# Optimization experiments

Measured on AMD Instinct MI355X. Metric: run time of the kernel, lower is better.

The kernel has to match this reference:

```python
import jax, jax.numpy as jnp
import numpy as np

B, L, F, H, DIM = 32, 1024, 1024, 1024, 1024


def setup_inputs() -> dict:
    key = jax.random.key(0)
    ks = jax.random.split(key, 8)
    features = jax.random.normal(ks[0], (B, L, F), dtype=jnp.float32)
    hidden = jax.random.normal(ks[1], (B, H), dtype=jnp.float32)
    # Dense layer params (glorot-ish scale)
    W1 = jax.random.normal(ks[2], (F, DIM), dtype=jnp.float32) / np.sqrt(F)
    b1 = jnp.zeros((DIM,), dtype=jnp.float32)
    W2 = jax.random.normal(ks[3], (H, DIM), dtype=jnp.float32) / np.sqrt(H)
    b2 = jnp.zeros((DIM,), dtype=jnp.float32)
    Wp = jax.random.normal(ks[4], (DIM, 1), dtype=jnp.float32) / np.sqrt(DIM)
    bp = jnp.zeros((1,), dtype=jnp.float32)
    return {"features": features, "hidden": hidden, "W1": W1, "b1": b1,
            "W2": W2, "b2": b2, "Wp": Wp, "bp": bp}


def reference(features, hidden, W1, b1, W2, b2, Wp, bp):
    # features: [B, L, F], hidden: [B, H]
    h1 = jnp.einsum('blf,fd->bld', features, W1) + b1          # [B, L, D]
    h2 = (hidden @ W2 + b2)[:, None, :]                         # [B, 1, D]
    att = jnp.tanh(h1 + h2)                                     # [B, L, D]
    score = jnp.einsum('bld,do->blo', att, Wp) + bp             # [B, L, 1]
    attention_weights = jax.nn.softmax(score, axis=1)           # [B, L, 1]
    context_vector = jnp.sum(attention_weights * features, axis=1)  # [B, F]
    return context_vector
```

## Files before the change

### kernel.cpp

```cpp
#include <hip/hip_runtime.h>
#include <hip/hip_bf16.h>


typedef __attribute__((ext_vector_type(8))) __bf16 bf16x8;
typedef __attribute__((ext_vector_type(4))) float f32x4;

#define BM 128
#define BN 128
#define BK 32
#define LDK 40

static __device__ __forceinline__ ushort f2bf(float x) {
  unsigned u = __float_as_uint(x);
  return (ushort)((u + 0x7fffu + ((u >> 16) & 1u)) >> 16);
}

typedef __attribute__((address_space(1))) void gbl_t;
typedef __attribute__((address_space(3))) void lds_t;
static __device__ __forceinline__ void gl_lds16(const void* g, void* l) {
  __builtin_amdgcn_global_load_lds((gbl_t*)g, (lds_t*)l, 16, 0, 0);
}

static __device__ __forceinline__ bf16x8 cvt8(float4 lo, float4 hi) {
  __hip_bfloat162 c0 = __float22bfloat162_rn({lo.x, lo.y});
  __hip_bfloat162 c1 = __float22bfloat162_rn({lo.z, lo.w});
  __hip_bfloat162 c2 = __float22bfloat162_rn({hi.x, hi.y});
  __hip_bfloat162 c3 = __float22bfloat162_rn({hi.z, hi.w});
  union { int4 i; bf16x8 v; } u;
  u.i.x = *(int*)&c0; u.i.y = *(int*)&c1; u.i.z = *(int*)&c2; u.i.w = *(int*)&c3;
  return u.v;
}

__global__ __launch_bounds__(256) void cvt_feat_kernel(
    const float* __restrict__ feat, ushort* __restrict__ featb) {
  const size_t i8 = ((size_t)blockIdx.x * 256 + threadIdx.x) * 8;
  float4 a = *(const float4*)(feat + i8);
  float4 b = *(const float4*)(feat + i8 + 4);
  ushort t[8];
  t[0] = f2bf(a.x); t[1] = f2bf(a.y); t[2] = f2bf(a.z); t[3] = f2bf(a.w);
  t[4] = f2bf(b.x); t[5] = f2bf(b.y); t[6] = f2bf(b.z); t[7] = f2bf(b.w);
  *(int4*)(featb + i8) = *(int4*)t;
}

__global__ __launch_bounds__(256) void transpose_w1_kernel(
    const float* __restrict__ W1, ushort* __restrict__ W1T) {
  __shared__ float t[64][65];
  const int tr = blockIdx.y, tc = blockIdx.x, tid = threadIdx.x;
  const int r = tid >> 4;
  const int c4 = (tid & 15) * 4;
#pragma unroll
  for (int p = 0; p < 4; ++p) {
    const int rr = p * 16 + r;
    float4 v = *(const float4*)(W1 + (size_t)(tr * 64 + rr) * 1024 + tc * 64 + c4);
    t[rr][c4] = v.x; t[rr][c4 + 1] = v.y; t[rr][c4 + 2] = v.z; t[rr][c4 + 3] = v.w;
  }
  __syncthreads();
  const int cc = tid >> 3;
  const int r8 = (tid & 7) * 8;
#pragma unroll
  for (int p = 0; p < 2; ++p) {
    const int c = p * 32 + cc;
    ushort tmp[8];
#pragma unroll
    for (int j = 0; j < 8; ++j) tmp[j] = f2bf(t[r8 + j][c]);
    *(int4*)(W1T + (size_t)(tc * 64 + c) * 1024 + tr * 64 + r8) = *(int4*)tmp;
  }
}

__global__ void zero_kernel(float* __restrict__ p) {
  p[(size_t)blockIdx.x * 256 + threadIdx.x] = 0.f;
}

__global__ __launch_bounds__(256) void h2_kernel(
    const float* __restrict__ hidden, const float* __restrict__ W2,
    const float* __restrict__ b2, float* __restrict__ h2p) {
  const int d = blockIdx.x * 256 + threadIdx.x;
  const int b = blockIdx.y;
  const int z = blockIdx.z;
  const int k0 = z * 128;
  __shared__ float h[128];
  if (threadIdx.x < 128) h[threadIdx.x] = hidden[b * 1024 + k0 + threadIdx.x];
  __syncthreads();
  float acc = (z == 0) ? b2[d] : 0.f;
#pragma unroll 8
  for (int k = 0; k < 128; ++k)
    acc += h[k] * W2[(size_t)(k0 + k) * 1024 + d];
  h2p[z * 32768 + b * 1024 + d] = acc;
}

#define GEMM_EPILOGUE(ROWG)                                                    \
  float hbv[4], wpv[4];                                                        \
  _Pragma("unroll") for (int j = 0; j < 4; ++j) {                              \
    const int d = col0 + wn * 64 + j * 16 + lrow;                              \
    float hv = b1[d];                                                          \
    _Pragma("unroll") for (int p = 0; p < 8; ++p)                              \
        hv += h2p[p * 32768 + b * 1024 + d];                                   \
    hbv[j] = hv;                                                               \
    wpv[j] = wp[d];                                                            \
  }                                                                            \
  float rsum[4][4];                                                            \
  _Pragma("unroll") for (int i = 0; i < 4; ++i) {                              \
    _Pragma("unroll") for (int r = 0; r < 4; ++r) {                            \
      float s = 0.f;                                                           \
      _Pragma("unroll") for (int j = 0; j < 4; ++j)                            \
          s += tanhf(acc[i][j][r] + hbv[j]) * wpv[j];                          \
      s += __shfl_xor(s, 8);                                                   \
      s += __shfl_xor(s, 4);                                                   \
      s += __shfl_xor(s, 2);                                                   \
      s += __shfl_xor(s, 1);                                                   \
      rsum[i][r] = s;                                                          \
    }                                                                          \
  }                                                                            \
  if (wn == 1 && lrow == 0) {                                                  \
    _Pragma("unroll") for (int i = 0; i < 4; ++i)                              \
        _Pragma("unroll") for (int r = 0; r < 4; ++r)                          \
            sred[wm][i * 16 + quad * 4 + r] = rsum[i][r];                      \
  }                                                                            \
  __syncthreads();                                                             \
  if (wn == 0 && lrow == 0) {                                                  \
    _Pragma("unroll") for (int i = 0; i < 4; ++i)                              \
        _Pragma("unroll") for (int r = 0; r < 4; ++r) {                        \
          const int ro = wm * 64 + i * 16 + quad * 4 + r;                      \
          score_p[(size_t)blockIdx.y * 32768 + (ROWG) + ro] =                  \
              rsum[i][r] + sred[wm][ro & 63];                                  \
        }                                                                      \
  }

__global__ __launch_bounds__(256) void gemm_score_bf16_kernel(
    const ushort* __restrict__ featb,
    const ushort* __restrict__ w1t,
    const float* __restrict__ b1, const float* __restrict__ h2p,
    const float* __restrict__ wp, float* __restrict__ score_p,
    int row_base) {
  __shared__ ushort ldsA[BM * BK];
  __shared__ ushort ldsB[BN * BK];
  __shared__ float sred[2][64];
  const int tid = threadIdx.x;
  const int row0 = blockIdx.x * BM;
  const int col0 = blockIdx.y * BN;
  const int b = (row_base + row0) >> 10;

  const int wave = tid >> 6, lane = tid & 63;
  const int wm = wave & 1, wn = wave >> 1;
  const int lrow = lane & 15, quad = lane >> 4;

  int a_go[2], b_go[2], ls[2];
#pragma unroll
  for (int it = 0; it < 2; ++it) {
    const int slot = wave * 128 + it * 64 + lane;
    const int r = slot >> 2, kc = slot & 3;
    const int swz = (r & 3) ^ ((r >> 2) & 3);
    a_go[it] = (row0 + r) * 1024 + (kc ^ swz) * 8;
    b_go[it] = (col0 + r) * 1024 + (kc ^ swz) * 8;
    ls[it] = (wave * 128 + it * 64) * 16;
  }

  f32x4 acc[4][4] = {};

  for (int k0 = 0; k0 < 1024; k0 += BK) {
#pragma unroll
    for (int it = 0; it < 2; ++it)
      gl_lds16(featb + a_go[it] + k0, (char*)ldsA + ls[it]);
#pragma unroll
    for (int it = 0; it < 2; ++it)
      gl_lds16(w1t + b_go[it] + k0, (char*)ldsB + ls[it]);
    __syncthreads();

    bf16x8 af[4], bfr[4];
#pragma unroll
    for (int i = 0; i < 4; ++i) {
      const int r = wm * 64 + i * 16 + lrow;
      const int swz = (r & 3) ^ ((r >> 2) & 3);
      af[i] = *(const bf16x8*)&ldsA[r * 32 + (quad ^ swz) * 8];
    }
#pragma unroll
    for (int j = 0; j < 4; ++j) {
      const int r = wn * 64 + j * 16 + lrow;
      const int swz = (r & 3) ^ ((r >> 2) & 3);
      bfr[j] = *(const bf16x8*)&ldsB[r * 32 + (quad ^ swz) * 8];
    }
#pragma unroll
    for (int i = 0; i < 4; ++i)
#pragma unroll
      for (int j = 0; j < 4; ++j)
        acc[i][j] = __builtin_amdgcn_mfma_f32_16x16x32_bf16(
            af[i], bfr[j], acc[i][j], 0, 0, 0);
    __syncthreads();
  }

  GEMM_EPILOGUE(row_base + row0)
}

__global__ __launch_bounds__(256) void gemm_score_cvt_kernel(
    const float* __restrict__ feat,
    const ushort* __restrict__ w1t, const float* __restrict__ b1,
    const float* __restrict__ h2p, const float* __restrict__ wp,
    float* __restrict__ score_p) {
  __shared__ ushort ldsA[BM * LDK];
  __shared__ ushort ldsB[BN * LDK];
  __shared__ float sred[2][64];
  const int tid = threadIdx.x;
  const int row0 = blockIdx.x * BM;
  const int col0 = blockIdx.y * BN;
  const int b = row0 >> 10;

  const int wave = tid >> 6, lane = tid & 63;
  const int wm = wave & 1, wn = wave >> 1;
  const int lrow = lane & 15, quad = lane >> 4;

  const int arow = tid >> 1;
  const int akof = (tid & 1) * 16;
  const int brow = tid >> 2;
  const int bkof = (tid & 3) * 8;

  f32x4 acc[4][4] = {};

  for (int k0 = 0; k0 < 1024; k0 += BK) {
    {
      const float* ap = feat + (size_t)(row0 + arow) * 1024 + k0 + akof;
      float4 v0 = *(const float4*)(ap + 0);
      float4 v1 = *(const float4*)(ap + 4);
      float4 v2 = *(const float4*)(ap + 8);
      float4 v3 = *(const float4*)(ap + 12);
      union { bf16x8 v; int4 i; } w0, w1;
      w0.v = cvt8(v0, v1);
      w1.v = cvt8(v2, v3);
      *(int4*)&ldsA[arow * LDK + akof] = w0.i;
      *(int4*)&ldsA[arow * LDK + akof + 8] = w1.i;
    }
#pragma unroll
    for (int p = 0; p < 2; ++p) {
      const int m = p * 64 + brow;
      *(int4*)&ldsB[m * LDK + bkof] =
          *(const int4*)(w1t + (size_t)(col0 + m) * 1024 + k0 + bkof);
    }
    __syncthreads();
    bf16x8 af[4], bfr[4];
#pragma unroll
    for (int i = 0; i < 4; ++i)
      af[i] = *(const bf16x8*)&ldsA[(wm * 64 + i * 16 + lrow) * LDK + quad * 8];
#pragma unroll
    for (int j = 0; j < 4; ++j)
      bfr[j] = *(const bf16x8*)&ldsB[(wn * 64 + j * 16 + lrow) * LDK + quad * 8];
#pragma unroll
    for (int i = 0; i < 4; ++i)
#pragma unroll
      for (int j = 0; j < 4; ++j)
        acc[i][j] = __builtin_amdgcn_mfma_f32_16x16x32_bf16(
            af[i], bfr[j], acc[i][j], 0, 0, 0);
    __syncthreads();
  }

  GEMM_EPILOGUE(row0)
}

__global__ __launch_bounds__(256) void softmax_kernel(
    const float* __restrict__ score_p, float* __restrict__ w) {
  const int b = blockIdx.x, tid = threadIdx.x;
  const int lane = tid & 63, wv = tid >> 6;
  __shared__ float sm[4], ss[4];
  float v[4];
  float mx = -1e30f;
#pragma unroll
  for (int i = 0; i < 4; ++i) {
    const int idx = b * 1024 + i * 256 + tid;
    float s = 0.f;
#pragma unroll
    for (int p = 0; p < 8; ++p) s += score_p[p * 32768 + idx];
    v[i] = s;
    mx = fmaxf(mx, s);
  }
#pragma unroll
  for (int off = 32; off; off >>= 1) mx = fmaxf(mx, __shfl_xor(mx, off));
  if (lane == 0) sm[wv] = mx;
  __syncthreads();
  mx = fmaxf(fmaxf(sm[0], sm[1]), fmaxf(sm[2], sm[3]));
  float sum = 0.f;
#pragma unroll
  for (int i = 0; i < 4; ++i) {
    v[i] = __expf(v[i] - mx);
    sum += v[i];
  }
#pragma unroll
  for (int off = 32; off; off >>= 1) sum += __shfl_xor(sum, off);
  if (lane == 0) ss[wv] = sum;
  __syncthreads();
  const float inv = 1.f / (ss[0] + ss[1] + ss[2] + ss[3]);
#pragma unroll
  for (int i = 0; i < 4; ++i) w[b * 1024 + i * 256 + tid] = v[i] * inv;
}

__global__ __launch_bounds__(256) void context_kernel(
    const float* __restrict__ w, const float* __restrict__ feat,
    float* __restrict__ out) {
  const int b = blockIdx.y;
  const int l0 = blockIdx.x * 32;
  const int f0 = threadIdx.x * 4;
  __shared__ float wl[32];
  if (threadIdx.x < 32) wl[threadIdx.x] = w[b * 1024 + l0 + threadIdx.x];
  __syncthreads();
  const float* fb = feat + (size_t)b * 1048576 + (size_t)l0 * 1024 + f0;
  float a0 = 0.f, a1 = 0.f, a2 = 0.f, a3 = 0.f;
#pragma unroll 8
  for (int l = 0; l < 32; ++l) {
    float4 v = *(const float4*)(fb + (size_t)l * 1024);
    const float wv = wl[l];
    a0 += wv * v.x;
    a1 += wv * v.y;
    a2 += wv * v.z;
    a3 += wv * v.w;
  }
  float* dst = out + b * 1024 + f0;
  atomicAdd(dst + 0, a0);
  atomicAdd(dst + 1, a1);
  atomicAdd(dst + 2, a2);
  atomicAdd(dst + 3, a3);
}

extern "C" void kernel_launch(void* const* d_in, const int* in_sizes, int n_in,
                              void* d_out, int out_size, void* d_ws, size_t ws_size,
                              hipStream_t stream) {
  const float* feat   = (const float*)d_in[0];
  const float* hidden = (const float*)d_in[1];
  const float* W1     = (const float*)d_in[2];
  const float* b1     = (const float*)d_in[3];
  const float* W2     = (const float*)d_in[4];
  const float* b2     = (const float*)d_in[5];
  const float* Wp     = (const float*)d_in[6];
  float* out = (float*)d_out;

  char* ws = (char*)d_ws;
  ushort* w1t    = (ushort*)ws;
  float* score_p = (float*)(ws + 2097152);
  float* h2p     = (float*)(ws + 3145728);
  float* wts     = (float*)(ws + 4194304);
  ushort* featb  = (ushort*)(ws + 4325376);
  const bool big_ws = ws_size >= (size_t)(4325376 + 33554432);

  transpose_w1_kernel<<<dim3(16, 16), 256, 0, stream>>>(W1, w1t);
  h2_kernel<<<dim3(4, 32, 8), 256, 0, stream>>>(hidden, W2, b2, h2p);

  if (big_ws) {
    for (int h = 0; h < 2; ++h) {
      cvt_feat_kernel<<<8192, 256, 0, stream>>>(feat + (size_t)h * 16777216,
                                                featb);
      gemm_score_bf16_kernel<<<dim3(128, 8), 256, 0, stream>>>(
          featb, w1t, b1, h2p, Wp, score_p, h * 16384);
    }
  } else {
    gemm_score_cvt_kernel<<<dim3(256, 8), 256, 0, stream>>>(feat, w1t, b1, h2p,
                                                            Wp, score_p);
  }

  softmax_kernel<<<32, 256, 0, stream>>>(score_p, wts);
  zero_kernel<<<128, 256, 0, stream>>>(out);
  context_kernel<<<dim3(32, 32), 256, 0, stream>>>(wts, feat, out);
}
```

Baseline: 373.4 us.

## Double GEMM K-tile to 64, use fast tanh, vectorize bf16 convert, widen context blocks

```diff
diff --git a/kernel.cpp b/kernel.cpp
--- a/kernel.cpp
+++ b/kernel.cpp
@@ -7,7 +7,6 @@
 
 #define BM 128
 #define BN 128
-#define BK 32
 #define LDK 40
 
 static __device__ __forceinline__ ushort f2bf(float x) {
@@ -31,15 +30,19 @@
   return u.v;
 }
 
+static __device__ __forceinline__ float tanh_fast(float x) {
+  float e = __expf(2.f * x);
+  return 1.f - 2.f / (e + 1.f);
+}
+
 __global__ __launch_bounds__(256) void cvt_feat_kernel(
     const float* __restrict__ feat, ushort* __restrict__ featb) {
   const size_t i8 = ((size_t)blockIdx.x * 256 + threadIdx.x) * 8;
   float4 a = *(const float4*)(feat + i8);
   float4 b = *(const float4*)(feat + i8 + 4);
-  ushort t[8];
-  t[0] = f2bf(a.x); t[1] = f2bf(a.y); t[2] = f2bf(a.z); t[3] = f2bf(a.w);
-  t[4] = f2bf(b.x); t[5] = f2bf(b.y); t[6] = f2bf(b.z); t[7] = f2bf(b.w);
-  *(int4*)(featb + i8) = *(int4*)t;
+  union { bf16x8 v; int4 i; } u;
+  u.v = cvt8(a, b);
+  *(int4*)(featb + i8) = u.i;
 }
 
 __global__ __launch_bounds__(256) void transpose_w1_kernel(
@@ -103,7 +106,7 @@
     _Pragma("unroll") for (int r = 0; r < 4; ++r) {                            \
       float s = 0.f;                                                           \
       _Pragma("unroll") for (int j = 0; j < 4; ++j)                            \
-          s += tanhf(acc[i][j][r] + hbv[j]) * wpv[j];                          \
+          s += tanh_fast(acc[i][j][r] + hbv[j]) * wpv[j];                      \
       s += __shfl_xor(s, 8);                                                   \
       s += __shfl_xor(s, 4);                                                   \
       s += __shfl_xor(s, 2);                                                   \
@@ -132,8 +135,8 @@
     const float* __restrict__ b1, const float* __restrict__ h2p,
     const float* __restrict__ wp, float* __restrict__ score_p,
     int row_base) {
-  __shared__ ushort ldsA[BM * BK];
-  __shared__ ushort ldsB[BN * BK];
+  __shared__ ushort ldsA[BM * 64];
+  __shared__ ushort ldsB[BN * 64];
   __shared__ float sred[2][64];
   const int tid = threadIdx.x;
   const int row0 = blockIdx.x * BM;
@@ -144,47 +147,48 @@
   const int wm = wave & 1, wn = wave >> 1;
   const int lrow = lane & 15, quad = lane >> 4;
 
-  int a_go[2], b_go[2], ls[2];
-#pragma unroll
-  for (int it = 0; it < 2; ++it) {
-    const int slot = wave * 128 + it * 64 + lane;
-    const int r = slot >> 2, kc = slot & 3;
-    const int swz = (r & 3) ^ ((r >> 2) & 3);
-    a_go[it] = (row0 + r) * 1024 + (kc ^ swz) * 8;
-    b_go[it] = (col0 + r) * 1024 + (kc ^ swz) * 8;
-    ls[it] = (wave * 128 + it * 64) * 16;
+  int a_go[4], b_go[4], ls[4];
+#pragma unroll
+  for (int it = 0; it < 4; ++it) {
+    const int slot = wave * 256 + it * 64 + lane;
+    const int r = slot >> 3, c = slot & 7;
+    const int gc = c ^ (r & 7);
+    a_go[it] = (row0 + r) * 1024 + gc * 8;
+    b_go[it] = (col0 + r) * 1024 + gc * 8;
+    ls[it] = (wave * 256 + it * 64) * 16;
   }
 
   f32x4 acc[4][4] = {};
 
-  for (int k0 = 0; k0 < 1024; k0 += BK) {
-#pragma unroll
-    for (int it = 0; it < 2; ++it)
+  for (int k0 = 0; k0 < 1024; k0 += 64) {
+#pragma unroll
+    for (int it = 0; it < 4; ++it)
       gl_lds16(featb + a_go[it] + k0, (char*)ldsA + ls[it]);
 #pragma unroll
-    for (int it = 0; it < 2; ++it)
+    for (int it = 0; it < 4; ++it)
       gl_lds16(w1t + b_go[it] + k0, (char*)ldsB + ls[it]);
     __syncthreads();
 
-    bf16x8 af[4], bfr[4];
-#pragma unroll
-    for (int i = 0; i < 4; ++i) {
-      const int r = wm * 64 + i * 16 + lrow;
-      const int swz = (r & 3) ^ ((r >> 2) & 3);
-      af[i] = *(const bf16x8*)&ldsA[r * 32 + (quad ^ swz) * 8];
+#pragma unroll
+    for (int s = 0; s < 2; ++s) {
+      bf16x8 af[4], bfr[4];
+#pragma unroll
+      for (int i = 0; i < 4; ++i) {
+        const int r = wm * 64 + i * 16 + lrow;
+        af[i] = *(const bf16x8*)&ldsA[r * 64 + (((s * 4 + quad) ^ (r & 7)) * 8)];
+      }
+#pragma unroll
+      for (int j = 0; j < 4; ++j) {
+        const int r = wn * 64 + j * 16 + lrow;
+        bfr[j] = *(const bf16x8*)&ldsB[r * 64 + (((s * 4 + quad) ^ (r & 7)) * 8)];
+      }
+#pragma unroll
+      for (int i = 0; i < 4; ++i)
+#pragma unroll
+        for (int j = 0; j < 4; ++j)
+          acc[i][j] = __builtin_amdgcn_mfma_f32_16x16x32_bf16(
+              af[i], bfr[j], acc[i][j], 0, 0, 0);
     }
-#pragma unroll
-    for (int j = 0; j < 4; ++j) {
-      const int r = wn * 64 + j * 16 + lrow;
-      const int swz = (r & 3) ^ ((r >> 2) & 3);
-      bfr[j] = *(const bf16x8*)&ldsB[r * 32 + (quad ^ swz) * 8];
-    }
-#pragma unroll
-    for (int i = 0; i < 4; ++i)
-#pragma unroll
-      for (int j = 0; j < 4; ++j)
-        acc[i][j] = __builtin_amdgcn_mfma_f32_16x16x32_bf16(
-            af[i], bfr[j], acc[i][j], 0, 0, 0);
     __syncthreads();
   }
 
@@ -192,10 +196,9 @@
 }
 
 __global__ __launch_bounds__(256) void gemm_score_cvt_kernel(
-    const float* __restrict__ feat,
-    const ushort* __restrict__ w1t, const float* __restrict__ b1,
-    const float* __restrict__ h2p, const float* __restrict__ wp,
-    float* __restrict__ score_p) {
+    const float* __restrict__ feat, const ushort* __restrict__ w1t,
+    const float* __restrict__ b1, const float* __restrict__ h2p,
+    const float* __restrict__ wp, float* __restrict__ score_p) {
   __shared__ ushort ldsA[BM * LDK];
   __shared__ ushort ldsB[BN * LDK];
   __shared__ float sred[2][64];
@@ -215,7 +218,7 @@
 
   f32x4 acc[4][4] = {};
 
-  for (int k0 = 0; k0 < 1024; k0 += BK) {
+  for (int k0 = 0; k0 < 1024; k0 += 32) {
     {
       const float* ap = feat + (size_t)(row0 + arow) * 1024 + k0 + akof;
       float4 v0 = *(const float4*)(ap + 0);
@@ -294,15 +297,15 @@
     const float* __restrict__ w, const float* __restrict__ feat,
     float* __restrict__ out) {
   const int b = blockIdx.y;
-  const int l0 = blockIdx.x * 32;
+  const int l0 = blockIdx.x * 64;
   const int f0 = threadIdx.x * 4;
-  __shared__ float wl[32];
-  if (threadIdx.x < 32) wl[threadIdx.x] = w[b * 1024 + l0 + threadIdx.x];
+  __shared__ float wl[64];
+  if (threadIdx.x < 64) wl[threadIdx.x] = w[b * 1024 + l0 + threadIdx.x];
   __syncthreads();
   const float* fb = feat + (size_t)b * 1048576 + (size_t)l0 * 1024 + f0;
   float a0 = 0.f, a1 = 0.f, a2 = 0.f, a3 = 0.f;
 #pragma unroll 8
-  for (int l = 0; l < 32; ++l) {
+  for (int l = 0; l < 64; ++l) {
     float4 v = *(const float4*)(fb + (size_t)l * 1024);
     const float wv = wl[l];
     a0 += wv * v.x;
@@ -354,5 +357,5 @@
 
   softmax_kernel<<<32, 256, 0, stream>>>(score_p, wts);
   zero_kernel<<<128, 256, 0, stream>>>(out);
-  context_kernel<<<dim3(32, 32), 256, 0, stream>>>(wts, feat, out);
-}
+  context_kernel<<<dim3(16, 32), 256, 0, stream>>>(wts, feat, out);
+}
```

New measurement: 347.0 us. 1.08x faster.
